# Performance work log

Hardware: AMD Instinct MI355X
Metric: run time of the kernel (lower is better)

The kernel has to match this reference:

```python
import jax, jax.numpy as jnp
import numpy as np
from jax import lax

D_MODEL, D_STATE, D_CONV, EXPAND = 1024, 16, 4, 2
D_INNER = EXPAND * D_MODEL
B, L = 2, 2048


def setup_inputs() -> dict:
    key = jax.random.key(0)
    ks = jax.random.split(key, 8)
    s_in = 1.0 / np.sqrt(D_MODEL)
    s_xp = 1.0 / np.sqrt(D_INNER)
    x = jax.random.normal(ks[0], (B, L, D_MODEL), dtype=jnp.float32)
    W_in = jax.random.uniform(ks[1], (2 * D_INNER, D_MODEL), minval=-s_in, maxval=s_in)
    conv_w = jax.random.uniform(ks[2], (D_INNER, 1, D_CONV), minval=-0.5, maxval=0.5)
    conv_b = jax.random.uniform(ks[3], (D_INNER,), minval=-0.5, maxval=0.5)
    W_xproj = jax.random.uniform(ks[4], (1 + 2 * D_STATE, D_INNER), minval=-s_xp, maxval=s_xp)
    W_dt = jax.random.uniform(ks[5], (D_INNER, 1), minval=-1.0, maxval=1.0)
    b_dt = jax.random.uniform(ks[6], (D_INNER,), minval=-1.0, maxval=1.0)
    A_log = jnp.log(jnp.broadcast_to(jnp.arange(1, D_STATE + 1, dtype=jnp.float32), (D_INNER, D_STATE)))
    D = jnp.ones((D_INNER,), dtype=jnp.float32)
    W_out = jax.random.uniform(ks[7], (D_MODEL, D_INNER), minval=-s_xp, maxval=s_xp)
    return {"x": x, "W_in": W_in, "conv_w": conv_w, "conv_b": conv_b,
            "W_xproj": W_xproj, "W_dt": W_dt, "b_dt": b_dt,
            "A_log": A_log, "D": D, "W_out": W_out}


def reference(x, W_in, conv_w, conv_b, W_xproj, W_dt, b_dt, A_log, D, W_out):
    b, l, _ = x.shape
    d_state = A_log.shape[1]
    d_conv = conv_w.shape[-1]

    xz = x @ W_in.T                                  # (B, L, 2*d_inner)
    x_in, z = jnp.split(xz, 2, axis=-1)

    # causal depthwise conv: torch pads both sides then truncates to [:L]
    lhs = jnp.pad(x_in.transpose(0, 2, 1), ((0, 0), (0, 0), (d_conv - 1, 0)))  # (B, d_inner, L+pad)
    conv = lax.conv_general_dilated(
        lhs, conv_w, window_strides=(1,), padding='VALID',
        dimension_numbers=('NCW', 'OIW', 'NCW'),
        feature_group_count=conv_w.shape[0])
    x_conv = jax.nn.silu(conv.transpose(0, 2, 1) + conv_b)  # (B, L, d_inner)

    ssm_in = x_conv @ W_xproj.T                      # (B, L, 1+2*d_state)
    dt_raw = ssm_in[..., :1]
    B_ssm = ssm_in[..., 1:1 + d_state]               # (B, L, d_state)
    C_ssm = ssm_in[..., 1 + d_state:]                # (B, L, d_state)

    delta = jax.nn.softplus(dt_raw @ W_dt.T + b_dt)  # (B, L, d_inner)
    A = -jnp.exp(A_log)                              # (d_inner, d_state)
    deltaA = jnp.exp(delta[..., None] * A)           # (B, L, d_inner, d_state)
    deltaB_u = delta[..., None] * B_ssm[:, :, None, :] * x_conv[..., None]

    def step(h, inp):
        dA, dBu, c = inp                              # (B,d_inner,d_state)x2, (B,d_state)
        h = dA * h + dBu
        y = jnp.einsum('bds,bs->bd', h, c)
        return h, y

    h0 = jnp.zeros((b, deltaA.shape[2], d_state), dtype=x.dtype)
    _, ys = lax.scan(step, h0, (deltaA.transpose(1, 0, 2, 3),
                                deltaB_u.transpose(1, 0, 2, 3),
                                C_ssm.transpose(1, 0, 2)))
    y = ys.transpose(1, 0, 2) + x_conv * D           # (B, L, d_inner)
    y = y * jax.nn.silu(z)
    return y @ W_out.T
```

## Files before the change

### kernel.cpp

```cpp
#include <hip/hip_runtime.h>
#include <hip/hip_bf16.h>
#include <math.h>

#define D_MODEL 1024
#define D_STATE 16
#define D_CONV  4
#define D_INNER 2048
#define BB      2
#define LL      2048
#define BLROWS  (BB*LL)
#define NCHUNK  64
#define CHUNK   (LL/NCHUNK)
#define SSML    36
#define XSPLIT  16

typedef __hip_bfloat16 bf16;
typedef __attribute__((ext_vector_type(8))) short short8;
typedef __attribute__((ext_vector_type(4))) float f32x4;

__device__ __forceinline__ float ldf(const void* p, long i, int isbf) {
    return isbf ? __bfloat162float(((const bf16*)p)[i]) : ((const float*)p)[i];
}
__device__ __forceinline__ short bfbits(float f) {
    bf16 h = __float2bfloat16(f);
    return *(short*)&h;
}
__device__ __forceinline__ float bits2f(short s) {
    bf16 h; *(short*)&h = s; return __bfloat162float(h);
}
__device__ __forceinline__ float bf2f(bf16 h) { return __bfloat162float(h); }
__device__ __forceinline__ float siluf(float x) {
    return __fdividef(x, 1.f + __expf(-x));
}
__device__ __forceinline__ void softplus_r(float x, float& delta, float& r) {
    float e = __expf(-fabsf(x));
    float t = 1.f + e;
    delta = fmaxf(x, 0.f) + __logf(t);
    r = __fdividef((x >= 0.f) ? e : 1.f, t);
}

#define OFF_CW   0
#define OFF_CB   8192
#define OFF_WDT  10240
#define OFF_BDT  12288
#define OFF_AA   14336
#define OFF_D    47104
#define N_SMALL  49152
#define N_WXPB   (128*2048)
#define N_SSMZ   (BLROWS*SSML)

#define G_LDS16(gptr, lptr) __builtin_amdgcn_global_load_lds( \
    (const __attribute__((address_space(1))) void*)(gptr),    \
    (__attribute__((address_space(3))) void*)(lptr), 16, 0, 0)

__global__ void dtype_probe(const unsigned short* __restrict__ alog, int* __restrict__ flag) {
    if (threadIdx.x == 0) { flag[0] = (alog[1] != 0) ? 1 : 0; flag[1] = 1; }
}

__global__ __launch_bounds__(256) void cvt_prep(
    const void* __restrict__ Wxp, const void* __restrict__ cw,
    const void* __restrict__ cb, const void* __restrict__ wdt,
    const void* __restrict__ bdt, const void* __restrict__ alog,
    const void* __restrict__ Dp,
    bf16* __restrict__ wxpb, float* __restrict__ smallf,
    float* __restrict__ ssm, int* __restrict__ flag)
{
    const int isbf = flag[0];
    int idx = blockIdx.x * 256 + threadIdx.x;
    if (idx < N_WXPB) {
        int row = idx >> 11, col = idx & 2047;
        float v = (row < 33) ? ldf(Wxp, (long)row*2048 + col, isbf) : 0.f;
        wxpb[idx] = __float2bfloat16(v);
        return;
    }
    int j = idx - N_WXPB;
    if      (j < 8192)  smallf[OFF_CW  + j]         = ldf(cw,  j, isbf);
    else if (j < 10240) smallf[OFF_CB  + j - 8192]  = ldf(cb,  j - 8192, isbf);
    else if (j < 12288) smallf[OFF_WDT + j - 10240] = ldf(wdt, j - 10240, isbf);
    else if (j < 14336) smallf[OFF_BDT + j - 12288] = ldf(bdt, j - 12288, isbf);
    else if (j < 47104) {
        int jj = j - 14336;
        float aa = -__expf(ldf(alog, jj, isbf));
        smallf[OFF_AA + jj] = aa;
        int s = jj & 15;
        if (fabsf(aa + (float)(s+1)) > 1e-3f) flag[1] = 0;
    }
    else if (j < 49152) smallf[OFF_D   + j - 47104] = ldf(Dp,  j - 47104, isbf);
    else {
        int z = j - N_SMALL;
        if (z < N_SSMZ) ssm[z] = 0.f;
    }
}

__global__ __launch_bounds__(256) void cvt_all(
    const void* __restrict__ x, const void* __restrict__ win,
    const void* __restrict__ wout,
    bf16* __restrict__ xb, bf16* __restrict__ winb, bf16* __restrict__ woutb,
    const int* __restrict__ flagp)
{
    const int isbf = *flagp;
    int i = blockIdx.x * 256 + threadIdx.x;
    const void* src; bf16* dst; long o;
    if (i < 524288)       { src = x;    dst = xb;    o = (long)i * 8; }
    else if (i < 1048576) { src = win;  dst = winb;  o = (long)(i - 524288) * 8; }
    else if (i < 1310720) { src = wout; dst = woutb; o = (long)(i - 1048576) * 8; }
    else return;
    short8 v;
    if (isbf) {
        v = *(const short8*)((const bf16*)src + o);
    } else {
        const float* s = (const float*)src + o;
        f32x4 u = *(const f32x4*)s, w = *(const f32x4*)(s + 4);
        v[0]=bfbits(u[0]); v[1]=bfbits(u[1]); v[2]=bfbits(u[2]); v[3]=bfbits(u[3]);
        v[4]=bfbits(w[0]); v[5]=bfbits(w[1]); v[6]=bfbits(w[2]); v[7]=bfbits(w[3]);
    }
    *(short8*)(dst + o) = v;
}

__global__ __launch_bounds__(512) void gemm8p(
    const bf16* __restrict__ A,
    const bf16* __restrict__ Bm,
    bf16* __restrict__ Cp)
{
    __shared__ bf16 As[2][256*64];
    __shared__ bf16 Bs[2][256*64];
    const int t    = threadIdx.x;
    const int lane = t & 63;
    const int wm   = (t >> 6) >> 2;
    const int wn   = (t >> 6) & 3;
    const int bm   = blockIdx.y, bn = blockIdx.x;
    const int quad = lane >> 4, l16 = lane & 15;
    const int NST  = 16;

    f32x4 acc[8][4];
    #pragma unroll
    for (int i = 0; i < 8; i++)
        #pragma unroll
        for (int j = 0; j < 4; j++)
            acc[i][j] = f32x4{0.f, 0.f, 0.f, 0.f};

    auto stage = [&](int bufi, int kt) {
        #pragma unroll
        for (int seg = 0; seg < 4; seg++) {
            int s = seg*512 + t, row = s >> 3, sg = s & 7;
            int col = (sg ^ (row & 7)) * 8;
            G_LDS16(A + ((long)bm*256 + row)*1024 + kt*64 + col, &As[bufi][s*8]);
        }
        #pragma unroll
        for (int seg = 0; seg < 4; seg++) {
            int s = seg*512 + t, row = s >> 3, sg = s & 7;
            int col = (sg ^ (row & 7)) * 8;
            G_LDS16(Bm + ((long)bn*256 + row)*1024 + kt*64 + col, &Bs[bufi][s*8]);
        }
    };

    stage(0, 0);
    stage(1, 1);
    asm volatile("s_waitcnt vmcnt(8)" ::: "memory");
    __builtin_amdgcn_s_barrier();

    int cur = 0;
    for (int t0 = 0; t0 < NST; ++t0) {
        short8 af[2][8], bfv[2][4];
        #pragma unroll
        for (int kk = 0; kk < 2; kk++) {
            #pragma unroll
            for (int rt = 0; rt < 8; rt++) {
                int row = wm*128 + rt*16 + l16;
                int c = kk*4 + quad;
                af[kk][rt] = *(const short8*)&As[cur][row*64 + ((c ^ (row & 7))*8)];
            }
            #pragma unroll
            for (int ct = 0; ct < 4; ct++) {
                int row = wn*64 + ct*16 + l16;
                int c = kk*4 + quad;
                bfv[kk][ct] = *(const short8*)&Bs[cur][row*64 + ((c ^ (row & 7))*8)];
            }
        }
        asm volatile("s_waitcnt lgkmcnt(0)" ::: "memory");
        __builtin_amdgcn_sched_barrier(0);
        __builtin_amdgcn_s_barrier();
        __builtin_amdgcn_sched_barrier(0);
        if (t0 + 2 < NST) stage(cur, t0 + 2);
        __builtin_amdgcn_s_setprio(1);
        #pragma unroll
        for (int kk = 0; kk < 2; kk++)
            #pragma unroll
            for (int rt = 0; rt < 8; rt++)
                #pragma unroll
                for (int ct = 0; ct < 4; ct++)
                    acc[rt][ct] = __builtin_amdgcn_mfma_f32_16x16x32_bf16(
                        af[kk][rt], bfv[kk][ct], acc[rt][ct], 0, 0, 0);
        __builtin_amdgcn_s_setprio(0);
        __builtin_amdgcn_sched_barrier(0);
        if (t0 + 2 < NST) { asm volatile("s_waitcnt vmcnt(8)" ::: "memory"); }
        else              { asm volatile("s_waitcnt vmcnt(0)" ::: "memory"); }
        __builtin_amdgcn_sched_barrier(0);
        __builtin_amdgcn_s_barrier();
        cur ^= 1;
    }

    #pragma unroll
    for (int rt = 0; rt < 8; rt++)
        #pragma unroll
        for (int ct = 0; ct < 4; ct++)
            #pragma unroll
            for (int r = 0; r < 4; r++) {
                int row = bm*256 + wm*128 + rt*16 + quad*4 + r;
                int col = bn*256 + wn*64 + ct*16 + l16;
                Cp[(long)row * 4096 + col] = __float2bfloat16(acc[rt][ct][r]);
            }
}

__global__ __launch_bounds__(256) void gemm_dual(
    const void* __restrict__ A, int lda,
    const void* __restrict__ Bm, int ldb,
    void* __restrict__ Cp, int ldc, int K,
    const int* __restrict__ flagp, int amode, int bmode, int cmode)
{
    const int isbf = *flagp;
    const int a_bf = amode ? isbf : 1;
    const int b_bf = bmode ? isbf : 1;
    const int c_bf = cmode ? isbf : 1;

    __shared__ bf16 As[128*64];
    __shared__ bf16 Bs[128*64];
    const int t    = threadIdx.x;
    const int lane = t & 63;
    const int w    = t >> 6;
    const int wm   = w >> 1, wn = w & 1;
    const int bm   = blockIdx.y, bn = blockIdx.x;
    const int quad = lane >> 4, l16 = lane & 15;

    f32x4 acc[4][4];
    #pragma unroll
    for (int i = 0; i < 4; i++)
        #pragma unroll
        for (int j = 0; j < 4; j++)
            acc[i][j] = f32x4{0.f, 0.f, 0.f, 0.f};

    for (int k0 = 0; k0 < K; k0 += 64) {
        __syncthreads();
        if (a_bf) {
            #pragma unroll
            for (int seg = 0; seg < 4; seg++) {
                int s = seg*256 + t, row = s >> 3, sg = s & 7;
                int col = (sg ^ (row & 7)) * 8;
                const bf16* ga = (const bf16*)A + ((long)bm*128 + row)*(long)lda + k0 + col;
                G_LDS16(ga, &As[row*64 + sg*8]);
            }
        } else {
            #pragma unroll
            for (int seg = 0; seg < 4; seg++) {
                int s = seg*256 + t, row = s >> 3, sg = s & 7;
                int col = (sg ^ (row & 7)) * 8;
                const float* ap = (const float*)A + ((long)bm*128 + row)*(long)lda + k0 + col;
                f32x4 u = *(const f32x4*)ap, v = *(const f32x4*)(ap + 4);
                short8 va;
                va[0]=bfbits(u[0]); va[1]=bfbits(u[1]); va[2]=bfbits(u[2]); va[3]=bfbits(u[3]);
                va[4]=bfbits(v[0]); va[5]=bfbits(v[1]); va[6]=bfbits(v[2]); va[7]=bfbits(v[3]);
                *(short8*)&As[row*64 + sg*8] = va;
            }
        }
        if (b_bf) {
            #pragma unroll
            for (int seg = 0; seg < 4; seg++) {
                int s = seg*256 + t, row = s >> 3, sg = s & 7;
                int col = (sg ^ (row & 7)) * 8;
                const bf16* gb = (const bf16*)Bm + ((long)bn*128 + row)*(long)ldb + k0 + col;
                G_LDS16(gb, &Bs[row*64 + sg*8]);
            }
        } else {
            #pragma unroll
            for (int seg = 0; seg < 4; seg++) {
                int s = seg*256 + t, row = s >> 3, sg = s & 7;
                int col = (sg ^ (row & 7)) * 8;
                const float* bp = (const float*)Bm + ((long)bn*128 + row)*(long)ldb + k0 + col;
                f32x4 u = *(const f32x4*)bp, v = *(const f32x4*)(bp + 4);
                short8 vb;
                vb[0]=bfbits(u[0]); vb[1]=bfbits(u[1]); vb[2]=bfbits(u[2]); vb[3]=bfbits(u[3]);
                vb[4]=bfbits(v[0]); vb[5]=bfbits(v[1]); vb[6]=bfbits(v[2]); vb[7]=bfbits(v[3]);
                *(short8*)&Bs[row*64 + sg*8] = vb;
            }
        }
        __syncthreads();

        #pragma unroll
        for (int kk = 0; kk < 64; kk += 32) {
            const int cbase = kk >> 3;
            short8 af[4], bfr[4];
            #pragma unroll
            for (int mi = 0; mi < 4; mi++) {
                int row = wm*64 + mi*16 + l16;
                int c = cbase + quad;
                af[mi] = *(const short8*)&As[row*64 + ((c ^ (row & 7))*8)];
            }
            #pragma unroll
            for (int ni = 0; ni < 4; ni++) {
                int row = wn*64 + ni*16 + l16;
                int c = cbase + quad;
                bfr[ni] = *(const short8*)&Bs[row*64 + ((c ^ (row & 7))*8)];
            }
            #pragma unroll
            for (int mi = 0; mi < 4; mi++)
                #pragma unroll
                for (int ni = 0; ni < 4; ni++)
                    acc[mi][ni] = __builtin_amdgcn_mfma_f32_16x16x32_bf16(
                        af[mi], bfr[ni], acc[mi][ni], 0, 0, 0);
        }
    }

    #pragma unroll
    for (int mi = 0; mi < 4; mi++)
        #pragma unroll
        for (int ni = 0; ni < 4; ni++)
            #pragma unroll
            for (int r = 0; r < 4; r++) {
                int row = bm*128 + wm*64 + mi*16 + quad*4 + r;
                int col = bn*128 + wn*64 + ni*16 + l16;
                float val = acc[mi][ni][r];
                if (c_bf) ((bf16*)Cp)[(long)row * ldc + col] = __float2bfloat16(val);
                else      ((float*)Cp)[(long)row * ldc + col] = val;
            }
}

__global__ __launch_bounds__(256) void gemm_n64(
    const bf16* __restrict__ A, int lda,
    const void* __restrict__ Bm, int ldb,
    void* __restrict__ Cp, int ldc, int K,
    const int* __restrict__ flagp, int bmode, int cmode)
{
    const int isbf = *flagp;
    const int b_bf = bmode ? isbf : 1;
    const int c_bf = cmode ? isbf : 1;

    __shared__ bf16 As[128*64];
    __shared__ bf16 Bs[64*64];
    const int t    = threadIdx.x;
    const int lane = t & 63;
    const int w    = t >> 6;
    const int wm   = w >> 1, wn = w & 1;
    const int bm   = blockIdx.y, bn = blockIdx.x;
    const int quad = lane >> 4, l16 = lane & 15;

    f32x4 acc[4][2];
    #pragma unroll
    for (int i = 0; i < 4; i++)
        #pragma unroll
        for (int j = 0; j < 2; j++)
            acc[i][j] = f32x4{0.f, 0.f, 0.f, 0.f};

    for (int k0 = 0; k0 < K; k0 += 64) {
        __syncthreads();
        #pragma unroll
        for (int seg = 0; seg < 4; seg++) {
            int s = seg*256 + t, row = s >> 3, sg = s & 7;
            int col = (sg ^ (row & 7)) * 8;
            const bf16* ga = A + ((long)bm*128 + row)*(long)lda + k0 + col;
            G_LDS16(ga, &As[row*64 + sg*8]);
        }
        if (b_bf) {
            #pragma unroll
            for (int seg = 0; seg < 2; seg++) {
                int s = seg*256 + t, row = s >> 3, sg = s & 7;
                int col = (sg ^ (row & 7)) * 8;
                const bf16* gb = (const bf16*)Bm + ((long)bn*64 + row)*(long)ldb + k0 + col;
                G_LDS16(gb, &Bs[row*64 + sg*8]);
            }
        } else {
            #pragma unroll
            for (int seg = 0; seg < 2; seg++) {
                int s = seg*256 + t, row = s >> 3, sg = s & 7;
                int col = (sg ^ (row & 7)) * 8;
                const float* bp = (const float*)Bm + ((long)bn*64 + row)*(long)ldb + k0 + col;
                f32x4 u = *(const f32x4*)bp, v = *(const f32x4*)(bp + 4);
                short8 vb;
                vb[0]=bfbits(u[0]); vb[1]=bfbits(u[1]); vb[2]=bfbits(u[2]); vb[3]=bfbits(u[3]);
                vb[4]=bfbits(v[0]); vb[5]=bfbits(v[1]); vb[6]=bfbits(v[2]); vb[7]=bfbits(v[3]);
                *(short8*)&Bs[row*64 + sg*8] = vb;
            }
        }
        __syncthreads();

        #pragma unroll
        for (int kk = 0; kk < 64; kk += 32) {
            const int cbase = kk >> 3;
            short8 af[4], bfr[2];
            #pragma unroll
            for (int mi = 0; mi < 4; mi++) {
                int row = wm*64 + mi*16 + l16;
                int c = cbase + quad;
                af[mi] = *(const short8*)&As[row*64 + ((c ^ (row & 7))*8)];
            }
            #pragma unroll
            for (int ni = 0; ni < 2; ni++) {
                int row = wn*32 + ni*16 + l16;
                int c = cbase + quad;
                bfr[ni] = *(const short8*)&Bs[row*64 + ((c ^ (row & 7))*8)];
            }
            #pragma unroll
            for (int mi = 0; mi < 4; mi++)
                #pragma unroll
                for (int ni = 0; ni < 2; ni++)
                    acc[mi][ni] = __builtin_amdgcn_mfma_f32_16x16x32_bf16(
                        af[mi], bfr[ni], acc[mi][ni], 0, 0, 0);
        }
    }

    #pragma unroll
    for (int mi = 0; mi < 4; mi++)
        #pragma unroll
        for (int ni = 0; ni < 2; ni++)
            #pragma unroll
            for (int r = 0; r < 4; r++) {
                int row = bm*128 + wm*64 + mi*16 + quad*4 + r;
                int col = bn*64 + wn*32 + ni*16 + l16;
                float val = acc[mi][ni][r];
                if (c_bf) ((bf16*)Cp)[(long)row * ldc + col] = __float2bfloat16(val);
                else      ((float*)Cp)[(long)row * ldc + col] = val;
            }
}

__global__ __launch_bounds__(256) void xproj_fused(
    const bf16* __restrict__ xz, const bf16* __restrict__ wxpb,
    const float* __restrict__ smallf, float* __restrict__ ssm,
    bf16* __restrict__ xcb)
{
    const float* cwf = smallf + OFF_CW;
    const float* cbf = smallf + OFF_CB;
    __shared__ bf16 As[128*32];
    __shared__ bf16 Bs[128*32];
    const int t    = threadIdx.x;
    const int lane = t & 63;
    const int w    = t >> 6;
    const int wm   = w >> 1, wn = w & 1;
    const int bm   = blockIdx.y;
    const int ks   = blockIdx.x * (D_INNER / XSPLIT);
    const int quad = lane >> 4, l16 = lane & 15;

    f32x4 acc[4][4];
    #pragma unroll
    for (int i = 0; i < 4; i++)
        #pragma unroll
        for (int j = 0; j < 4; j++)
            acc[i][j] = f32x4{0.f, 0.f, 0.f, 0.f};

    for (int k0 = ks; k0 < ks + D_INNER/XSPLIT; k0 += 32) {
        __syncthreads();
        #pragma unroll
        for (int seg = 0; seg < 2; seg++) {
            int s = seg*256 + t, row = s >> 2, dcol = (s & 3) * 8;
            int blg = bm*128 + row;
            int b = blg >> 11, l = blg & (LL - 1);
            int d0 = k0 + dcol;
            float a[8];
            {
                f32x4 c0 = *(const f32x4*)&cbf[d0], c1 = *(const f32x4*)&cbf[d0+4];
                a[0]=c0[0]; a[1]=c0[1]; a[2]=c0[2]; a[3]=c0[3];
                a[4]=c1[0]; a[5]=c1[1]; a[6]=c1[2]; a[7]=c1[3];
            }
            f32x4 cw4[8];
            #pragma unroll
            for (int j = 0; j < 8; j++) cw4[j] = *(const f32x4*)&cwf[(d0+j)*4];
            #pragma unroll
            for (int kk = 0; kk < D_CONV; kk++) {
                int ls = l - 3 + kk;
                if (ls >= 0) {
                    short8 xv = *(const short8*)&xz[((long)(b*LL + ls))*4096 + d0];
                    #pragma unroll
                    for (int j = 0; j < 8; j++) a[j] += bits2f(xv[j]) * cw4[j][kk];
                }
            }
            short8 va;
            #pragma unroll
            for (int j = 0; j < 8; j++) va[j] = bfbits(siluf(a[j]));
            *(short8*)&As[row*32 + dcol] = va;
            if (xcb) *(short8*)&xcb[(long)blg*D_INNER + d0] = va;
        }
        #pragma unroll
        for (int seg = 0; seg < 2; seg++) {
            int s = seg*256 + t, row = s >> 2, col = (s & 3) * 8;
            const bf16* gb = wxpb + (long)row*D_INNER + k0 + col;
            G_LDS16(gb, &Bs[row*32 + col]);
        }
        __syncthreads();

        short8 af[4], bfr[4];
        #pragma unroll
        for (int mi = 0; mi < 4; mi++)
            af[mi] = *(const short8*)&As[(wm*64 + mi*16 + l16)*32 + quad*8];
        #pragma unroll
        for (int ni = 0; ni < 4; ni++)
            bfr[ni] = *(const short8*)&Bs[(wn*64 + ni*16 + l16)*32 + quad*8];
        #pragma unroll
        for (int mi = 0; mi < 4; mi++)
            #pragma unroll
            for (int ni = 0; ni < 4; ni++)
                acc[mi][ni] = __builtin_amdgcn_mfma_f32_16x16x32_bf16(
                    af[mi], bfr[ni], acc[mi][ni], 0, 0, 0);
    }

    #pragma unroll
    for (int mi = 0; mi < 4; mi++)
        #pragma unroll
        for (int ni = 0; ni < 4; ni++) {
            int col = wn*64 + ni*16 + l16;
            if (col < 33) {
                int newcol = (col == 0) ? 32 : (col - 1);
                #pragma unroll
                for (int r = 0; r < 4; r++) {
                    int row = bm*128 + wm*64 + mi*16 + quad*4 + r;
                    atomicAdd(&ssm[(long)row * SSML + newcol], acc[mi][ni][r]);
                }
            }
        }
}

template<int CHUNK_T>
__global__ __launch_bounds__(256) void scan_partA(
    const float* __restrict__ ssm, const bf16* __restrict__ xz,
    const float* __restrict__ smallf,
    float* __restrict__ sumdq, float* __restrict__ Q,
    const int* __restrict__ flag)
{
    __shared__ float sL[CHUNK_T*SSML];
    __shared__ bf16  sX[CHUNK_T*256];
    const int fastA = flag[1];
    int d = blockIdx.x * 256 + threadIdx.x;
    int c = blockIdx.y, b = blockIdx.z;
    const int NC = gridDim.y;
    int l0 = c * CHUNK_T;
    {
        const float* src = ssm + (long)(b*LL + l0) * SSML;
        for (int idx = threadIdx.x; idx < CHUNK_T*SSML; idx += 256) sL[idx] = src[idx];
        const bf16* xsrc = xz + (long)(b*LL + l0)*4096 + blockIdx.x*256;
        for (int j = threadIdx.x; j < CHUNK_T*32; j += 256) {
            int li = j >> 5, ln = j & 31;
            *(short8*)&sX[li*256 + ln*8] = *(const short8*)&xsrc[(long)li*4096 + ln*8];
        }
    }
    f32x4 h4[4];
    #pragma unroll
    for (int g = 0; g < 4; g++) h4[g] = f32x4{0.f, 0.f, 0.f, 0.f};
    float Aa[D_STATE];
    if (!fastA) {
        #pragma unroll
        for (int s = 0; s < D_STATE; s++) Aa[s] = smallf[OFF_AA + d*D_STATE + s];
    }
    f32x4 cw4 = *(const f32x4*)&smallf[OFF_CW + d*4];
    float cbv  = smallf[OFF_CB + d];
    float wdt  = smallf[OFF_WDT + d];
    float bdtv = smallf[OFF_BDT + d];
    float win[3];
    #pragma unroll
    for (int k = 0; k < 3; k++) {
        int ls = l0 - 3 + k;
        win[k] = (ls >= 0) ? bf2f(xz[((long)(b*LL + ls))*4096 + d]) : 0.f;
    }
    __syncthreads();
    float sumd = 0.f;
    #pragma unroll 4
    for (int li = 0; li < CHUNK_T; li++) {
        float xnew = bf2f(sX[li*256 + threadIdx.x]);
        float convv = cbv + win[0]*cw4[0] + win[1]*cw4[1] + win[2]*cw4[2] + xnew*cw4[3];
        win[0] = win[1]; win[1] = win[2]; win[2] = xnew;
        float xc = siluf(convv);
        const float* row = &sL[li*SSML];
        f32x4 Bv[4];
        #pragma unroll
        for (int g = 0; g < 4; g++) Bv[g] = *(const f32x4*)(row + g*4);
        float delta, r;
        softplus_r(row[32]*wdt + bdtv, delta, r);
        sumd += delta;
        float du = delta * xc;
        if (fastA) {
            float r2 = r*r, r3 = r2*r, r4 = r2*r2;
            f32x4 p0; p0[0]=r; p0[1]=r2; p0[2]=r3; p0[3]=r4;
            float s8 = r4*r4, s12 = s8*r4;
            h4[0] = p0*h4[0]       + du*Bv[0];
            h4[1] = (p0*r4)*h4[1]  + du*Bv[1];
            h4[2] = (p0*s8)*h4[2]  + du*Bv[2];
            h4[3] = (p0*s12)*h4[3] + du*Bv[3];
        } else {
            #pragma unroll
            for (int g = 0; g < 4; g++)
                #pragma unroll
                for (int j = 0; j < 4; j++) {
                    int s = g*4 + j;
                    h4[g][j] = __expf(delta*Aa[s])*h4[g][j] + du*Bv[g][j];
                }
        }
    }
    sumdq[(long)(b*NC + c)*D_INNER + d] = sumd;
    long o = ((long)(b*NC + c)*D_STATE)*D_INNER + d;
    #pragma unroll
    for (int s = 0; s < D_STATE; s++)
        Q[o + (long)s*D_INNER] = h4[s >> 2][s & 3];
}

template<int CHUNK_T>
__global__ __launch_bounds__(256) void scan_partA_xc(
    const float* __restrict__ ssm, const bf16* __restrict__ xcb,
    const float* __restrict__ smallf,
    float* __restrict__ sumdq, float* __restrict__ Q,
    const int* __restrict__ flag)
{
    __shared__ float sL[CHUNK_T*SSML];
    __shared__ bf16  sX[CHUNK_T*256];
    const int fastA = flag[1];
    int d = blockIdx.x * 256 + threadIdx.x;
    int c = blockIdx.y, b = blockIdx.z;
    const int NC = gridDim.y;
    int l0 = c * CHUNK_T;
    {
        const float* src = ssm + (long)(b*LL + l0) * SSML;
        for (int idx = threadIdx.x; idx < CHUNK_T*SSML; idx += 256) sL[idx] = src[idx];
        const bf16* xsrc = xcb + (long)(b*LL + l0)*D_INNER + blockIdx.x*256;
        for (int j = threadIdx.x; j < CHUNK_T*32; j += 256) {
            int li = j >> 5, ln = j & 31;
            *(short8*)&sX[li*256 + ln*8] = *(const short8*)&xsrc[(long)li*D_INNER + ln*8];
        }
    }
    f32x4 h4[4];
    #pragma unroll
    for (int g = 0; g < 4; g++) h4[g] = f32x4{0.f, 0.f, 0.f, 0.f};
    float Aa[D_STATE];
    if (!fastA) {
        #pragma unroll
        for (int s = 0; s < D_STATE; s++) Aa[s] = smallf[OFF_AA + d*D_STATE + s];
    }
    float wdt  = smallf[OFF_WDT + d];
    float bdtv = smallf[OFF_BDT + d];
    __syncthreads();
    float sumd = 0.f;
    #pragma unroll 4
    for (int li = 0; li < CHUNK_T; li++) {
        float xc = bf2f(sX[li*256 + threadIdx.x]);
        const float* row = &sL[li*SSML];
        f32x4 Bv[4];
        #pragma unroll
        for (int g = 0; g < 4; g++) Bv[g] = *(const f32x4*)(row + g*4);
        float delta, r;
        softplus_r(row[32]*wdt + bdtv, delta, r);
        sumd += delta;
        float du = delta * xc;
        if (fastA) {
            float r2 = r*r, r3 = r2*r, r4 = r2*r2;
            f32x4 p0; p0[0]=r; p0[1]=r2; p0[2]=r3; p0[3]=r4;
            float s8 = r4*r4, s12 = s8*r4;
            h4[0] = p0*h4[0]       + du*Bv[0];
            h4[1] = (p0*r4)*h4[1]  + du*Bv[1];
            h4[2] = (p0*s8)*h4[2]  + du*Bv[2];
            h4[3] = (p0*s12)*h4[3] + du*Bv[3];
        } else {
            #pragma unroll
            for (int g = 0; g < 4; g++)
                #pragma unroll
                for (int j = 0; j < 4; j++) {
                    int s = g*4 + j;
                    h4[g][j] = __expf(delta*Aa[s])*h4[g][j] + du*Bv[g][j];
                }
        }
    }
    sumdq[(long)(b*NC + c)*D_INNER + d] = sumd;
    long o = ((long)(b*NC + c)*D_STATE)*D_INNER + d;
    #pragma unroll
    for (int s = 0; s < D_STATE; s++)
        Q[o + (long)s*D_INNER] = h4[s >> 2][s & 3];
}

__global__ __launch_bounds__(256) void scan_combine(
    const float* __restrict__ sumdq, float* __restrict__ Q_hst,
    const float* __restrict__ smallf, int NC)
{
    int t = blockIdx.x * 256 + threadIdx.x;
    int d = t & (D_INNER - 1);
    int s = (t >> 11) & (D_STATE - 1);
    int b = t >> 15;
    float Aa = smallf[OFF_AA + d*D_STATE + s];
    float h = 0.f;
    #pragma unroll 4
    for (int c = 0; c < NC; c++) {
        float sd = sumdq[(long)(b*NC + c)*D_INNER + d];
        long idx = ((long)(b*NC + c)*D_STATE + s)*D_INNER + d;
        float q = Q_hst[idx];
        Q_hst[idx] = h;
        h = __expf(Aa*sd)*h + q;
    }
}

template<int CHUNK_T>
__global__ __launch_bounds__(256) void scan_partC(
    const float* __restrict__ ssm, bf16* __restrict__ xz,
    const float* __restrict__ smallf, const float* __restrict__ hst,
    const int* __restrict__ flag)
{
    __shared__ float sL[CHUNK_T*SSML];
    __shared__ bf16  sX[CHUNK_T*256];
    __shared__ bf16  sZ[CHUNK_T*256];
    const int fastA = flag[1];
    int d = blockIdx.x * 256 + threadIdx.x;
    int c = blockIdx.y, b = blockIdx.z;
    const int NC = gridDim.y;
    int l0 = c * CHUNK_T;
    {
        const float* src = ssm + (long)(b*LL + l0) * SSML;
        for (int idx = threadIdx.x; idx < CHUNK_T*SSML; idx += 256) sL[idx] = src[idx];
        const bf16* xsrc = xz + (long)(b*LL + l0)*4096 + blockIdx.x*256;
        for (int j = threadIdx.x; j < CHUNK_T*32; j += 256) {
            int li = j >> 5, ln = j & 31;
            *(short8*)&sX[li*256 + ln*8] = *(const short8*)&xsrc[(long)li*4096 + ln*8];
            *(short8*)&sZ[li*256 + ln*8] = *(const short8*)&xsrc[(long)li*4096 + D_INNER + ln*8];
        }
    }
    f32x4 h4[4];
    long o = ((long)(b*NC + c)*D_STATE)*D_INNER + d;
    #pragma unroll
    for (int s = 0; s < D_STATE; s++) h4[s >> 2][s & 3] = hst[o + (long)s*D_INNER];
    float Aa[D_STATE];
    if (!fastA) {
        #pragma unroll
        for (int s = 0; s < D_STATE; s++) Aa[s] = smallf[OFF_AA + d*D_STATE + s];
    }
    f32x4 cw4 = *(const f32x4*)&smallf[OFF_CW + d*4];
    float cbv  = smallf[OFF_CB + d];
    float wdt  = smallf[OFF_WDT + d];
    float bdtv = smallf[OFF_BDT + d];
    float Dv   = smallf[OFF_D + d];
    float win[3];
    #pragma unroll
    for (int k = 0; k < 3; k++) {
        int ls = l0 - 3 + k;
        win[k] = (ls >= 0) ? bf2f(xz[((long)(b*LL + ls))*4096 + d]) : 0.f;
    }
    __syncthreads();
    #pragma unroll 2
    for (int li = 0; li < CHUNK_T; li++) {
        long bl = (long)(b*LL + l0 + li);
        float xnew = bf2f(sX[li*256 + threadIdx.x]);
        float convv = cbv + win[0]*cw4[0] + win[1]*cw4[1] + win[2]*cw4[2] + xnew*cw4[3];
        win[0] = win[1]; win[1] = win[2]; win[2] = xnew;
        float xc = siluf(convv);
        const float* row = &sL[li*SSML];
        f32x4 Bv[4], Cv[4];
        #pragma unroll
        for (int g = 0; g < 4; g++) {
            Bv[g] = *(const f32x4*)(row + g*4);
            Cv[g] = *(const f32x4*)(row + 16 + g*4);
        }
        float delta, r;
        softplus_r(row[32]*wdt + bdtv, delta, r);
        float du = delta * xc;
        f32x4 yacc = f32x4{0.f, 0.f, 0.f, 0.f};
        if (fastA) {
            float r2 = r*r, r3 = r2*r, r4 = r2*r2;
            f32x4 p0; p0[0]=r; p0[1]=r2; p0[2]=r3; p0[3]=r4;
            float s8 = r4*r4, s12 = s8*r4;
            h4[0] = p0*h4[0]       + du*Bv[0];
            h4[1] = (p0*r4)*h4[1]  + du*Bv[1];
            h4[2] = (p0*s8)*h4[2]  + du*Bv[2];
            h4[3] = (p0*s12)*h4[3] + du*Bv[3];
            yacc = yacc + h4[0]*Cv[0];
            yacc = yacc + h4[1]*Cv[1];
            yacc = yacc + h4[2]*Cv[2];
            yacc = yacc + h4[3]*Cv[3];
        } else {
            #pragma unroll
            for (int g = 0; g < 4; g++)
                #pragma unroll
                for (int j = 0; j < 4; j++) {
                    int s = g*4 + j;
                    h4[g][j] = __expf(delta*Aa[s])*h4[g][j] + du*Bv[g][j];
                    yacc[j] += h4[g][j]*Cv[g][j];
                }
        }
        float yv = (yacc[0] + yacc[1]) + (yacc[2] + yacc[3]);
        yv += xc * Dv;
        float z = bf2f(sZ[li*256 + threadIdx.x]);
        yv *= siluf(z);
        xz[bl*4096 + D_INNER + d] = __float2bfloat16(yv);
    }
}

template<int CHUNK_T>
__global__ __launch_bounds__(256) void scan_partC_xc(
    const float* __restrict__ ssm, bf16* __restrict__ xz,
    const bf16* __restrict__ xcb,
    const float* __restrict__ smallf, const float* __restrict__ hst,
    const int* __restrict__ flag)
{
    __shared__ float sL[CHUNK_T*SSML];
    __shared__ bf16  sX[CHUNK_T*256];
    __shared__ bf16  sZ[CHUNK_T*256];
    const int fastA = flag[1];
    int d = blockIdx.x * 256 + threadIdx.x;
    int c = blockIdx.y, b = blockIdx.z;
    const int NC = gridDim.y;
    int l0 = c * CHUNK_T;
    {
        const float* src = ssm + (long)(b*LL + l0) * SSML;
        for (int idx = threadIdx.x; idx < CHUNK_T*SSML; idx += 256) sL[idx] = src[idx];
        const bf16* xcs = xcb + (long)(b*LL + l0)*D_INNER + blockIdx.x*256;
        const bf16* zs  = xz  + (long)(b*LL + l0)*4096 + D_INNER + blockIdx.x*256;
        for (int j = threadIdx.x; j < CHUNK_T*32; j += 256) {
            int li = j >> 5, ln = j & 31;
            *(short8*)&sX[li*256 + ln*8] = *(const short8*)&xcs[(long)li*D_INNER + ln*8];
            *(short8*)&sZ[li*256 + ln*8] = *(const short8*)&zs[(long)li*4096 + ln*8];
        }
    }
    f32x4 h4[4];
    long o = ((long)(b*NC + c)*D_STATE)*D_INNER + d;
    #pragma unroll
    for (int s = 0; s < D_STATE; s++) h4[s >> 2][s & 3] = hst[o + (long)s*D_INNER];
    float Aa[D_STATE];
    if (!fastA) {
        #pragma unroll
        for (int s = 0; s < D_STATE; s++) Aa[s] = smallf[OFF_AA + d*D_STATE + s];
    }
    float wdt  = smallf[OFF_WDT + d];
    float bdtv = smallf[OFF_BDT + d];
    float Dv   = smallf[OFF_D + d];
    __syncthreads();
    #pragma unroll 2
    for (int li = 0; li < CHUNK_T; li++) {
        long bl = (long)(b*LL + l0 + li);
        float xc = bf2f(sX[li*256 + threadIdx.x]);
        const float* row = &sL[li*SSML];
        f32x4 Bv[4], Cv[4];
        #pragma unroll
        for (int g = 0; g < 4; g++) {
            Bv[g] = *(const f32x4*)(row + g*4);
            Cv[g] = *(const f32x4*)(row + 16 + g*4);
        }
        float delta, r;
        softplus_r(row[32]*wdt + bdtv, delta, r);
        float du = delta * xc;
        f32x4 yacc = f32x4{0.f, 0.f, 0.f, 0.f};
        if (fastA) {
            float r2 = r*r, r3 = r2*r, r4 = r2*r2;
            f32x4 p0; p0[0]=r; p0[1]=r2; p0[2]=r3; p0[3]=r4;
            float s8 = r4*r4, s12 = s8*r4;
            h4[0] = p0*h4[0]       + du*Bv[0];
            h4[1] = (p0*r4)*h4[1]  + du*Bv[1];
            h4[2] = (p0*s8)*h4[2]  + du*Bv[2];
            h4[3] = (p0*s12)*h4[3] + du*Bv[3];
            yacc = yacc + h4[0]*Cv[0];
            yacc = yacc + h4[1]*Cv[1];
            yacc = yacc + h4[2]*Cv[2];
            yacc = yacc + h4[3]*Cv[3];
        } else {
            #pragma unroll
            for (int g = 0; g < 4; g++)
                #pragma unroll
                for (int j = 0; j < 4; j++) {
                    int s = g*4 + j;
                    h4[g][j] = __expf(delta*Aa[s])*h4[g][j] + du*Bv[g][j];
                    yacc[j] += h4[g][j]*Cv[g][j];
                }
        }
        float yv = (yacc[0] + yacc[1]) + (yacc[2] + yacc[3]);
        yv += xc * Dv;
        float z = bf2f(sZ[li*256 + threadIdx.x]);
        yv *= siluf(z);
        xz[bl*4096 + D_INNER + d] = __float2bfloat16(yv);
    }
}

extern "C" void kernel_launch(void* const* d_in, const int* in_sizes, int n_in,
                              void* d_out, int out_size, void* d_ws, size_t ws_size,
                              hipStream_t stream)
{
    char* ws = (char*)d_ws;
    bf16*  xz     = (bf16*) (ws);
    bf16*  wxpb   = (bf16*) (ws + 33554432);
    float* ssm    = (float*)(ws + 34078720);
    float* sumdq  = (float*)(ws + 34668544);
    float* Q      = (float*)(ws + 35717120);
    float* smallf = (float*)(ws + 52494336);
    int*   flag   = (int*)  (ws + 52690944);
    bf16*  woutb  = (bf16*) (ws + 52691008);
    bf16*  xcb    = (bf16*) (ws + 56885312);
    bf16*  xb     = (bf16*) (ws + 35717120);
    bf16*  winb   = (bf16*) (ws + 35717120 + 8388608);
    const bool big  = ws_size >= 56885312;
    const bool big2 = ws_size >= 73662528;

    dtype_probe<<<1, 64, 0, stream>>>((const unsigned short*)d_in[7], flag);

    cvt_prep<<<(N_WXPB + N_SMALL + N_SSMZ)/256, 256, 0, stream>>>(
        d_in[4], d_in[2], d_in[3], d_in[5], d_in[6], d_in[7], d_in[8],
        wxpb, smallf, ssm, flag);

    if (big) {
        cvt_all<<<1310720/256, 256, 0, stream>>>(
            d_in[0], d_in[1], d_in[9], xb, winb, woutb, flag);
        gemm8p<<<dim3(16, 16), 512, 0, stream>>>(xb, winb, xz);
    } else {
        gemm_dual<<<dim3(32, 32), 256, 0, stream>>>(
            d_in[0], D_MODEL, d_in[1], D_MODEL, xz, 2*D_INNER, D_MODEL, flag, 1, 1, 0);
    }

    xproj_fused<<<dim3(XSPLIT, 32), 256, 0, stream>>>(
        xz, wxpb, smallf, ssm, big2 ? xcb : (bf16*)nullptr);

    {
        dim3 g(D_INNER/256, NCHUNK, BB);
        if (big2) {
            scan_partA_xc<CHUNK><<<g, 256, 0, stream>>>(ssm, xcb, smallf, sumdq, Q, flag);
            scan_combine<<<(BB*D_STATE*D_INNER)/256, 256, 0, stream>>>(sumdq, Q, smallf, NCHUNK);
            scan_partC_xc<CHUNK><<<g, 256, 0, stream>>>(ssm, xz, xcb, smallf, Q, flag);
        } else {
            scan_partA<CHUNK><<<g, 256, 0, stream>>>(ssm, xz, smallf, sumdq, Q, flag);
            scan_combine<<<(BB*D_STATE*D_INNER)/256, 256, 0, stream>>>(sumdq, Q, smallf, NCHUNK);
            scan_partC<CHUNK><<<g, 256, 0, stream>>>(ssm, xz, smallf, Q, flag);
        }
    }

    if (big) {
        gemm_n64<<<dim3(D_MODEL/64, 32), 256, 0, stream>>>(
            xz + D_INNER, 2*D_INNER, woutb, D_INNER, d_out, D_MODEL, D_INNER, flag, 0, 1);
    } else {
        gemm_n64<<<dim3(D_MODEL/64, 32), 256, 0, stream>>>(
            xz + D_INNER, 2*D_INNER, d_in[9], D_INNER, d_out, D_MODEL, D_INNER, flag, 1, 1);
    }
}
```

Measured before the change: 281.5 us.

## Restructure input GEMM into quadrant-split 8-wave pipeline with finer-grained staging

Replaces the 256x256 tile GEMM with a variant that splits the tile into four 128x128 quadrants. Each wave computes a 64x32 piece of every quadrant, and the global-to-LDS loads for half-tiles are interleaved between quadrant MFMA phases. The aim is to overlap memory loads with MFMA work at finer granularity and to reduce the register footprint of the fragments held live at once. In exchange there are more barriers per K step, and the vmcnt bookkeeping is more complex and could be fragile.

```diff
diff --git a/kernel.cpp b/kernel.cpp
--- a/kernel.cpp
+++ b/kernel.cpp
@@ -117,99 +117,118 @@
     *(short8*)(dst + o) = v;
 }
 
-__global__ __launch_bounds__(512) void gemm8p(
+__global__ __launch_bounds__(512) void gemm8x(
     const bf16* __restrict__ A,
     const bf16* __restrict__ Bm,
     bf16* __restrict__ Cp)
 {
-    __shared__ bf16 As[2][256*64];
-    __shared__ bf16 Bs[2][256*64];
+    __shared__ bf16 As[2][2][128*64];
+    __shared__ bf16 Bs[2][2][128*64];
     const int t    = threadIdx.x;
     const int lane = t & 63;
-    const int wm   = (t >> 6) >> 2;
-    const int wn   = (t >> 6) & 3;
+    const int w    = t >> 6;
+    const int rm   = w >> 2;
+    const int cn   = w & 3;
     const int bm   = blockIdx.y, bn = blockIdx.x;
     const int quad = lane >> 4, l16 = lane & 15;
-    const int NST  = 16;
-
-    f32x4 acc[8][4];
-    #pragma unroll
-    for (int i = 0; i < 8; i++)
-        #pragma unroll
-        for (int j = 0; j < 4; j++)
-            acc[i][j] = f32x4{0.f, 0.f, 0.f, 0.f};
-
-    auto stage = [&](int bufi, int kt) {
-        #pragma unroll
-        for (int seg = 0; seg < 4; seg++) {
+    const int NT   = 16;
+
+    f32x4 acc[4][4][2];
+    #pragma unroll
+    for (int p = 0; p < 4; p++)
+        #pragma unroll
+        for (int i = 0; i < 4; i++)
+            #pragma unroll
+            for (int j = 0; j < 2; j++)
+                acc[p][i][j] = f32x4{0.f, 0.f, 0.f, 0.f};
+
+    auto stageA = [&](int bufi, int half, int kt) {
+        #pragma unroll
+        for (int seg = 0; seg < 2; seg++) {
             int s = seg*512 + t, row = s >> 3, sg = s & 7;
             int col = (sg ^ (row & 7)) * 8;
-            G_LDS16(A + ((long)bm*256 + row)*1024 + kt*64 + col, &As[bufi][s*8]);
-        }
-        #pragma unroll
-        for (int seg = 0; seg < 4; seg++) {
+            G_LDS16(A + ((long)bm*256 + half*128 + row)*1024 + kt*64 + col,
+                    &As[bufi][half][s*8]);
+        }
+    };
+    auto stageB = [&](int bufi, int half, int kt) {
+        #pragma unroll
+        for (int seg = 0; seg < 2; seg++) {
             int s = seg*512 + t, row = s >> 3, sg = s & 7;
             int col = (sg ^ (row & 7)) * 8;
-            G_LDS16(Bm + ((long)bn*256 + row)*1024 + kt*64 + col, &Bs[bufi][s*8]);
+            G_LDS16(Bm + ((long)bn*256 + half*128 + row)*1024 + kt*64 + col,
+                    &Bs[bufi][half][s*8]);
         }
     };
 
-    stage(0, 0);
-    stage(1, 1);
-    asm volatile("s_waitcnt vmcnt(8)" ::: "memory");
+    stageA(0, 0, 0); stageB(0, 0, 0); stageA(0, 1, 0); stageB(0, 1, 0);
+    stageA(1, 0, 1); stageB(1, 0, 1);
+    asm volatile("s_waitcnt vmcnt(4)" ::: "memory");
     __builtin_amdgcn_s_barrier();
 
-    int cur = 0;
-    for (int t0 = 0; t0 < NST; ++t0) {
-        short8 af[2][8], bfv[2][4];
-        #pragma unroll
-        for (int kk = 0; kk < 2; kk++) {
-            #pragma unroll
-            for (int rt = 0; rt < 8; rt++) {
-                int row = wm*128 + rt*16 + l16;
-                int c = kk*4 + quad;
-                af[kk][rt] = *(const short8*)&As[cur][row*64 + ((c ^ (row & 7))*8)];
-            }
-            #pragma unroll
-            for (int ct = 0; ct < 4; ct++) {
-                int row = wn*64 + ct*16 + l16;
-                int c = kk*4 + quad;
-                bfv[kk][ct] = *(const short8*)&Bs[cur][row*64 + ((c ^ (row & 7))*8)];
-            }
-        }
-        asm volatile("s_waitcnt lgkmcnt(0)" ::: "memory");
-        __builtin_amdgcn_sched_barrier(0);
-        __builtin_amdgcn_s_barrier();
-        __builtin_amdgcn_sched_barrier(0);
-        if (t0 + 2 < NST) stage(cur, t0 + 2);
-        __builtin_amdgcn_s_setprio(1);
-        #pragma unroll
-        for (int kk = 0; kk < 2; kk++)
-            #pragma unroll
-            for (int rt = 0; rt < 8; rt++)
-                #pragma unroll
-                for (int ct = 0; ct < 4; ct++)
-                    acc[rt][ct] = __builtin_amdgcn_mfma_f32_16x16x32_bf16(
-                        af[kk][rt], bfv[kk][ct], acc[rt][ct], 0, 0, 0);
-        __builtin_amdgcn_s_setprio(0);
-        __builtin_amdgcn_sched_barrier(0);
-        if (t0 + 2 < NST) { asm volatile("s_waitcnt vmcnt(8)" ::: "memory"); }
-        else              { asm volatile("s_waitcnt vmcnt(0)" ::: "memory"); }
-        __builtin_amdgcn_sched_barrier(0);
-        __builtin_amdgcn_s_barrier();
-        cur ^= 1;
-    }
-
-    #pragma unroll
-    for (int rt = 0; rt < 8; rt++)
-        #pragma unroll
-        for (int ct = 0; ct < 4; ct++)
-            #pragma unroll
-            for (int r = 0; r < 4; r++) {
-                int row = bm*256 + wm*128 + rt*16 + quad*4 + r;
-                int col = bn*256 + wn*64 + ct*16 + l16;
-                Cp[(long)row * 4096 + col] = __float2bfloat16(acc[rt][ct][r]);
-            }
+    for (int kt = 0; kt < NT; ++kt) {
+        const int buf = kt & 1;
+        #pragma unroll
+        for (int p = 0; p < 4; ++p) {
+            const int qm = p >> 1, qn = p & 1;
+            short8 af[4][2], bfv[2][2];
+            #pragma unroll
+            for (int fi = 0; fi < 4; fi++)
+                #pragma unroll
+                for (int kk = 0; kk < 2; kk++) {
+                    int ar = rm*64 + fi*16 + l16;
+                    int c = kk*4 + quad;
+                    af[fi][kk] = *(const short8*)&As[buf][qm][ar*64 + ((c ^ (ar & 7))*8)];
+                }
+            #pragma unroll
+            for (int fj = 0; fj < 2; fj++)
+                #pragma unroll
+                for (int kk = 0; kk < 2; kk++) {
+                    int br = cn*32 + fj*16 + l16;
+                    int c = kk*4 + quad;
+                    bfv[fj][kk] = *(const short8*)&Bs[buf][qn][br*64 + ((c ^ (br & 7))*8)];
+                }
+            if      (p == 0) { if (kt + 1 < NT) stageA(buf ^ 1, 1, kt + 1); }
+            else if (p == 1) { if (kt + 1 < NT) stageB(buf ^ 1, 1, kt + 1); }
+            else if (p == 2) { if (kt + 2 < NT) stageA(buf, 0, kt + 2); }
+            else             { if (kt + 2 < NT) stageB(buf, 0, kt + 2); }
+            __builtin_amdgcn_s_barrier();
+            asm volatile("s_waitcnt lgkmcnt(0)" ::: "memory");
+            __builtin_amdgcn_sched_barrier(0);
+            __builtin_amdgcn_s_setprio(1);
+            #pragma unroll
+            for (int kk = 0; kk < 2; kk++)
+                #pragma unroll
+                for (int fi = 0; fi < 4; fi++)
+                    #pragma unroll
+                    for (int fj = 0; fj < 2; fj++)
+                        acc[p][fi][fj] = __builtin_amdgcn_mfma_f32_16x16x32_bf16(
+                            af[fi][kk], bfv[fj][kk], acc[p][fi][fj], 0, 0, 0);
+            __builtin_amdgcn_s_setprio(0);
+            __builtin_amdgcn_sched_barrier(0);
+            if (p == 3) {
+                if (kt == NT - 2)     { asm volatile("s_waitcnt vmcnt(0)" ::: "memory"); }
+                else if (kt < NT - 2) { asm volatile("s_waitcnt vmcnt(4)" ::: "memory"); }
+            }
+            __builtin_amdgcn_sched_barrier(0);
+            __builtin_amdgcn_s_barrier();
+        }
+    }
+
+    #pragma unroll
+    for (int p = 0; p < 4; p++) {
+        const int qm = p >> 1, qn = p & 1;
+        #pragma unroll
+        for (int fi = 0; fi < 4; fi++)
+            #pragma unroll
+            for (int fj = 0; fj < 2; fj++)
+                #pragma unroll
+                for (int r = 0; r < 4; r++) {
+                    int row = bm*256 + qm*128 + rm*64 + fi*16 + quad*4 + r;
+                    int col = bn*256 + qn*128 + cn*32 + fj*16 + l16;
+                    Cp[(long)row * 4096 + col] = __float2bfloat16(acc[p][fi][fj][r]);
+                }
+    }
 }
 
 __global__ __launch_bounds__(256) void gemm_dual(
@@ -894,7 +913,7 @@
     if (big) {
         cvt_all<<<1310720/256, 256, 0, stream>>>(
             d_in[0], d_in[1], d_in[9], xb, winb, woutb, flag);
-        gemm8p<<<dim3(16, 16), 512, 0, stream>>>(xb, winb, xz);
+        gemm8x<<<dim3(16, 16), 512, 0, stream>>>(xb, winb, xz);
     } else {
         gemm_dual<<<dim3(32, 32), 256, 0, stream>>>(
             d_in[0], D_MODEL, d_in[1], D_MODEL, xz, 2*D_INNER, D_MODEL, flag, 1, 1, 0);
```

After: 291.3 us. 3.5% more time.
